# Kernel tuning notes

Hardware: AMD Instinct MI355X
Metric: run time of the kernel (lower is better)

Reference implementation:

```python
import jax, jax.numpy as jnp
import numpy as np

B, C, V, K, H, W = 1, 3, 9, 8, 512, 512


def setup_inputs() -> dict:
    key = jax.random.key(0)
    k0, k1 = jax.random.split(key, 2)
    x = jax.random.normal(k0, (B, C, K, H, W), jnp.float32)          # FDL layers (spatial)
    y_views = jax.random.normal(k1, (B, C, V, H, W), jnp.float32)    # observed views (spatial)
    g = jnp.arange(3, dtype=jnp.float32) - 1.0                       # 3x3 camera grid positions
    uu, vv = jnp.meshgrid(g, g, indexing='ij')
    u = uu.reshape(-1)
    v = vv.reshape(-1)
    d = jnp.linspace(-2.0, 2.0, K).astype(jnp.float32)               # d_fdl disparities
    rho = jnp.full((1,), 0.3, jnp.float32)
    return {"x": x, "y_views": y_views, "u": u, "v": v, "d": d, "rho": rho}


def _pack_half_spectrum(Xf, x_c, y_c, n_proc):
    # [..., H, W] -> transpose to [..., W, H], center-roll so zero freq is at (x_c-1, y_c-1),
    # flatten x-major, keep the non-redundant half spectrum (first n_proc entries).
    Xt = jnp.swapaxes(Xf, -1, -2)
    Xt = jnp.roll(Xt, shift=(x_c - 1, y_c - 1), axis=(-2, -1))
    sh = Xt.shape
    return Xt.reshape(sh[:-2] + (sh[-2] * sh[-1],))[..., :n_proc]


def reference(x, y_views, u, v, d, rho):
    Bn, Cn, Kn = x.shape[0], x.shape[1], x.shape[2]
    Hn, Wn = x.shape[-2], x.shape[-1]
    rho = rho.reshape(())
    x_c = (Wn + 2) // 2                      # ceil((W+1)/2)
    y_c = (Hn + 2) // 2
    n_proc = Hn * (x_c - 1) + y_c            # half-spectrum size
    e0 = 1 - Hn % 2
    e1 = 1 - Wn % 2

    X = jnp.fft.fft2(x)                      # [B,C,K,H,W] complex64
    Y = jnp.fft.fft2(y_views)                # [B,C,V,H,W] complex64
    Xp = jnp.moveaxis(_pack_half_spectrum(X, x_c, y_c, n_proc), 2, 3) * rho   # [B,C,F,K]
    Yp = jnp.moveaxis(_pack_half_spectrum(Y, x_c, y_c, n_proc), 2, 3)         # [B,C,F,V]

    # centered angular frequency grids, flattened x-major to match packing order
    wx = (jnp.arange(Wn, dtype=jnp.float32) - (x_c - 1)) * (2.0 * np.pi / Wn)
    wy = (jnp.arange(Hn, dtype=jnp.float32) - (y_c - 1)) * (2.0 * np.pi / Hn)
    wx_f = jnp.repeat(wx, Hn)[:n_proc]       # [F]
    wy_f = jnp.tile(wy, Wn)[:n_proc]         # [F]

    # FDL data matrix A[f,v,k] = exp(i * d_k * (u_v*wx_f + v_v*wy_f))
    shift = u[None, :] * wx_f[:, None] + v[None, :] * wy_f[:, None]   # [F,V]
    A = jnp.exp(1j * shift[:, :, None] * d[None, None, :])            # [F,V,K] complex64
    Ah = jnp.conj(A)
    ATA = jnp.einsum('fvk,fvl->fkl', Ah, A)                           # [F,K,K]
    ATb = jnp.einsum('fvk,bcfv->bcfk', Ah, Yp)                        # [B,C,F,K]
    M = ATA + rho * jnp.eye(Kn, dtype=ATA.dtype)
    fdl = jnp.linalg.solve(M, (ATb + Xp)[..., None])[..., 0]          # [B,C,F,K]

    # pad redundant half with zeros, restore [B,C,K,H,W] layout
    fdl = jnp.pad(fdl, ((0, 0), (0, 0), (0, Hn * Wn - n_proc), (0, 0)))
    fdl = fdl.reshape(Bn, Cn, Wn, Hn, Kn).transpose(0, 1, 4, 3, 2)    # [B,C,K,H,W]

    # Hermitian (conjugate) symmetry reconstruction
    fdl = fdl.at[..., y_c:, x_c - 1:].set(jnp.conj(fdl[..., e0:y_c - 1, e1:x_c][..., ::-1, ::-1]))
    fdl = fdl.at[..., e0:y_c, x_c:].set(jnp.conj(fdl[..., y_c - 1:, e1:x_c - 1][..., ::-1, ::-1]))
    fdl = jnp.roll(fdl, shift=(1 - y_c, 1 - x_c), axis=(-2, -1))
    return jnp.fft.ifft2(fdl).real
```

## Files before the change

kernel.cpp:

```cpp
#include <hip/hip_runtime.h>
#include <math.h>

constexpr int N    = 512;
constexpr int LOGN = 9;
constexpr int NN   = N * N;
constexpr int CCH  = 3;
constexpr int KK   = 8;
constexpr int VV   = 9;
constexpr int FHALF = N * (N / 2) + (N / 2 + 1);
constexpr float PI_F = 3.14159265358979323846f;

__device__ __forceinline__ float2 cmulf(float2 a, float2 b) {
    return make_float2(a.x * b.x - a.y * b.y, a.x * b.y + a.y * b.x);
}
__device__ __forceinline__ float2 cadd(float2 a, float2 b) { return make_float2(a.x + b.x, a.y + b.y); }
__device__ __forceinline__ float2 csub(float2 a, float2 b) { return make_float2(a.x - b.x, a.y - b.y); }

template<int SG>
__device__ __forceinline__ float2 cmuli(float2 z) {
    return (SG < 0) ? make_float2(z.y, -z.x) : make_float2(-z.y, z.x);
}

template<int SG>
__device__ __forceinline__ void dft8(float2 x[8]) {
    const float c = 0.70710678118654752440f;
    float2 a0 = cadd(x[0], x[4]), a1 = cadd(x[1], x[5]);
    float2 a2 = cadd(x[2], x[6]), a3 = cadd(x[3], x[7]);
    float2 d0 = csub(x[0], x[4]), d1 = csub(x[1], x[5]);
    float2 d2 = csub(x[2], x[6]), d3 = csub(x[3], x[7]);
    float2 b0 = d0;
    float2 b1 = cmulf(d1, make_float2(c, (float)SG * c));
    float2 b2 = cmuli<SG>(d2);
    float2 b3 = cmulf(d3, make_float2(-c, (float)SG * c));
    float2 aa0 = cadd(a0, a2), aa1 = cadd(a1, a3);
    float2 ab0 = csub(a0, a2), ab1 = cmuli<SG>(csub(a1, a3));
    float2 ba0 = cadd(b0, b2), ba1 = cadd(b1, b3);
    float2 bb0 = csub(b0, b2), bb1 = cmuli<SG>(csub(b1, b3));
    x[0] = cadd(aa0, aa1); x[4] = csub(aa0, aa1);
    x[2] = cadd(ab0, ab1); x[6] = csub(ab0, ab1);
    x[1] = cadd(ba0, ba1); x[5] = csub(ba0, ba1);
    x[3] = cadd(bb0, bb1); x[7] = csub(bb0, bb1);
}

__device__ __forceinline__ void twiddle8(float2 v[8], float base) {
    float sn, cs;
    __sincosf(base, &sn, &cs);
    float2 w1 = make_float2(cs, sn);
    float2 wk = w1;
    v[1] = cmulf(v[1], wk);
    #pragma unroll
    for (int k = 2; k < 8; ++k) { wk = cmulf(wk, w1); v[k] = cmulf(v[k], wk); }
}

template<int SG>
__device__ __forceinline__ void wave_fft512(float2 v[8], float* sre, float* sim,
                                            int t, int stride, int off) {
    int t1 = t >> 3, t0 = t & 7;
    dft8<SG>(v);
    twiddle8(v, (float)SG * (2.0f * PI_F / 512.0f) * (float)t);
    #pragma unroll
    for (int k = 0; k < 8; ++k) {
        int a = (68 * k + 8 * t1 + t0) * stride + off;
        sre[a] = v[k].x; sim[a] = v[k].y;
    }
    #pragma unroll
    for (int n = 0; n < 8; ++n) {
        int a = (68 * t1 + 8 * n + t0) * stride + off;
        v[n] = make_float2(sre[a], sim[a]);
    }
    dft8<SG>(v);
    twiddle8(v, (float)SG * (2.0f * PI_F / 64.0f) * (float)t0);
    #pragma unroll
    for (int k = 0; k < 8; ++k) {
        int a = (68 * t0 + 8 * k + t1) * stride + off;
        sre[a] = v[k].x; sim[a] = v[k].y;
    }
    #pragma unroll
    for (int n = 0; n < 8; ++n) {
        int a = (68 * n + 8 * t0 + t1) * stride + off;
        v[n] = make_float2(sre[a], sim[a]);
    }
    dft8<SG>(v);
}

__global__ __launch_bounds__(256) void k_fft_r2c_rows_pack(const float* __restrict__ inx,
                                                           const float* __restrict__ iny,
                                                           int nximg,
                                                           float2* __restrict__ out) {
    __shared__ float sre[4][544];
    __shared__ float sim[4][544];
    int w = threadIdx.x >> 6, t = threadIdx.x & 63;
    long long gp = (long long)blockIdx.x * 4 + w;
    long long row0 = gp * 2;
    long long xrows = (long long)nximg * N;
    const float* src0 = (row0 < xrows) ? (inx + row0 * N)
                                       : (iny + (row0 - xrows) * N);
    const float* src1 = src0 + N;
    float2 v[8];
    #pragma unroll
    for (int e = 0; e < 8; ++e) v[e] = make_float2(src0[t + 64 * e], src1[t + 64 * e]);
    wave_fft512<-1>(v, sre[w], sim[w], t, 1, 0);
    int kb = (t >> 3) + 8 * (t & 7);
    #pragma unroll
    for (int k0 = 0; k0 < 8; ++k0) {
        int p = kb + 64 * k0;
        sre[w][p] = v[k0].x; sim[w][p] = v[k0].y;
    }
    float2* dst0 = out + row0 * N;
    float2* dst1 = dst0 + N;
    #pragma unroll
    for (int k0 = 4; k0 < 8; ++k0) {
        int p  = kb + 64 * k0;
        int mp = 512 - p;
        float zmx = sre[w][mp], zmy = sim[w][mp];
        float2 Zp = v[k0];
        dst0[p] = make_float2(0.5f * (Zp.x + zmx), 0.5f * (Zp.y - zmy));
        dst1[p] = make_float2(0.5f * (Zp.y + zmy), 0.5f * (zmx - Zp.x));
    }
    if (t == 0) {
        dst0[0] = make_float2(v[0].x, 0.0f);
        dst1[0] = make_float2(v[0].y, 0.0f);
    }
}

__global__ __launch_bounds__(256) void k_fft_r2c_rows(const float* __restrict__ in,
                                                      float2* __restrict__ out) {
    __shared__ float sre[4][544];
    __shared__ float sim[4][544];
    int w = threadIdx.x >> 6, t = threadIdx.x & 63;
    long long grow = (long long)blockIdx.x * 4 + w;
    const float* src = in + grow * N;
    float2 v[8];
    #pragma unroll
    for (int e = 0; e < 8; ++e) v[e] = make_float2(src[t + 64 * e], 0.0f);
    wave_fft512<-1>(v, sre[w], sim[w], t, 1, 0);
    float2* dst = out + grow * N;
    int kb = (t >> 3) + 8 * (t & 7);
    #pragma unroll
    for (int k0 = 0; k0 < 8; ++k0) dst[kb + 64 * k0] = v[k0];
}

template<int SG>
__global__ __launch_bounds__(256) void k_fft_pairswap(float2* __restrict__ data,
                                                      float scale, int lex, int sex) {
    __shared__ float sre[4][544];
    __shared__ float sim[4][544];
    int w = threadIdx.x >> 6, t = threadIdx.x & 63;
    int b = blockIdx.x;
    long long imgBase = (long long)(b >> 7) * NN;
    int pa = (b & 127) << 1;
    int rowg = pa + (w & 1) + ((w >> 1) << 8);
    const float2* src = data + imgBase + (long long)rowg * N;
    float2 v[8];
    #pragma unroll
    for (int e = 0; e < 8; ++e) v[e] = src[t + 64 * (e ^ lex)];
    __syncthreads();
    wave_fft512<SG>(v, sre[w], sim[w], t, 1, 0);
    float2* dst = data + imgBase + (long long)(rowg ^ 256) * N;
    int kb = (t >> 3) + 8 * (t & 7);
    #pragma unroll
    for (int k0 = 0; k0 < 8; ++k0) {
        float2 z = v[k0];
        dst[kb + 64 * (k0 ^ sex)] = make_float2(z.x * scale, z.y * scale);
    }
}

__global__ __launch_bounds__(256) void k_fft_cols_fwd(const float2* __restrict__ in,
                                                      float2* __restrict__ out) {
    __shared__ float tre[4896];
    __shared__ float tim[4896];
    int t = threadIdx.x;
    long long imgOff = (long long)blockIdx.y * NN;
    int bx = blockIdx.x;
    int x0 = bx ? (248 + (bx << 3)) : 0;
    {
        int xi2 = (t & 3) << 1;
        int yb  = t >> 2;
        const float2* img = in + imgOff;
        #pragma unroll
        for (int it = 0; it < 8; ++it) {
            int y = it * 64 + yb;
            float4 q = *(const float4*)&img[(long long)y * N + x0 + xi2];
            int a = y * 9 + xi2;
            tre[a] = q.x; tim[a] = q.y; tre[a + 1] = q.z; tim[a + 1] = q.w;
        }
    }
    __syncthreads();
    int w = t >> 6, lane = t & 63;
    int kb = (lane >> 3) + 8 * (lane & 7);
    #pragma unroll
    for (int r = 0; r < 2; ++r) {
        int cc = (w << 1) | r;
        if (bx == 0 && cc != 0) continue;
        float2 v[8];
        #pragma unroll
        for (int e = 0; e < 8; ++e) {
            int a = (lane + 64 * e) * 9 + cc;
            v[e] = make_float2(tre[a], tim[a]);
        }
        wave_fft512<-1>(v, tre, tim, lane, 9, cc);
        #pragma unroll
        for (int k0 = 0; k0 < 8; ++k0) {
            int a = (kb + 64 * k0) * 9 + cc;
            tre[a] = v[k0].x; tim[a] = v[k0].y;
        }
    }
    __syncthreads();
    {
        int xi = t >> 5, co = t & 31;
        if (!(bx == 0 && xi != 0)) {
            float2* orow = out + imgOff + (long long)((x0 + xi) ^ 256) * N;
            #pragma unroll
            for (int it = 0; it < 8; ++it) {
                int b = it * 64 + co * 2;
                int y1 = b ^ 256;
                int a1 = y1 * 9 + xi, a2 = (y1 + 1) * 9 + xi;
                *(float4*)&orow[b] = make_float4(tre[a1], tim[a1], tre[a2], tim[a2]);
            }
        }
    }
}

__device__ __forceinline__ void accum_pair(float2 bacc[KK], float tr[KK], float s,
                                           float d0, float dlt, float2 Yp, float2 Yn) {
    float2 Sp = make_float2(Yp.x + Yn.x, Yp.y + Yn.y);
    float2 Dm = make_float2(Yp.x - Yn.x, Yp.y - Yn.y);
    float sn, cs;
    __sincosf(s * d0, &sn, &cs);  float2 p = make_float2(cs, sn);
    __sincosf(s * dlt, &sn, &cs); float2 q = make_float2(cs, sn);
    float2 w = q;
    #pragma unroll
    for (int k = 0; k < KK; ++k) {
        bacc[k].x += p.x * Sp.x + p.y * Dm.y;
        bacc[k].y += p.x * Sp.y - p.y * Dm.x;
        if (k < KK - 1) {
            p = cmulf(p, q);
            tr[k + 1] += 2.0f * w.x;
            w = cmulf(w, q);
        }
    }
}

__device__ __forceinline__ void solve_point(float2 bacc[KK], float tr[KK], float rho) {
    float diag = tr[0] + rho;
    float L[36], Li[KK];
    #pragma unroll
    for (int j = 0; j < KK; ++j) {
        float acc = diag;
        #pragma unroll
        for (int t = 0; t < j; ++t) { float l = L[(j * (j - 1)) / 2 + t]; acc -= l * l; }
        float dj = sqrtf(acc);
        float inv = 1.0f / dj;
        Li[j] = inv;
        #pragma unroll
        for (int i = j + 1; i < KK; ++i) {
            float a = tr[i - j];
            #pragma unroll
            for (int t = 0; t < j; ++t)
                a -= L[(i * (i - 1)) / 2 + t] * L[(j * (j - 1)) / 2 + t];
            L[(i * (i - 1)) / 2 + j] = a * inv;
        }
    }
    #pragma unroll
    for (int i = 0; i < KK; ++i) {
        float2 a = bacc[i];
        #pragma unroll
        for (int t = 0; t < i; ++t) {
            float l = L[(i * (i - 1)) / 2 + t];
            a.x -= l * bacc[t].x;
            a.y -= l * bacc[t].y;
        }
        bacc[i] = make_float2(a.x * Li[i], a.y * Li[i]);
    }
    #pragma unroll
    for (int i = KK - 1; i >= 0; --i) {
        float2 a = bacc[i];
        #pragma unroll
        for (int t = i + 1; t < KK; ++t) {
            float l = L[(t * (t - 1)) / 2 + i];
            a.x -= l * bacc[t].x;
            a.y -= l * bacc[t].y;
        }
        bacc[i] = make_float2(a.x * Li[i], a.y * Li[i]);
    }
}

__global__ __launch_bounds__(256) void k_solve_ifft(const float2* __restrict__ Xs,
                                                    const float2* __restrict__ Ys,
                                                    float2* __restrict__ P,
                                                    float2* __restrict__ S0,
                                                    const float* __restrict__ uu,
                                                    const float* __restrict__ vv,
                                                    const float* __restrict__ dd,
                                                    const float* __restrict__ rhop) {
    __shared__ float gre[KK][N];
    __shared__ float gim[KK][N];
    __shared__ float fsre[4][544];
    __shared__ float fsim[4][544];
    int a  = blockIdx.x;
    int ch = blockIdx.y;
    int t  = threadIdx.x;
    float rho = rhop[0];
    float d0 = dd[0], dlt = dd[1] - dd[0];
    const float C = 2.0f * PI_F / (float)N;
    float wxv = (float)(a - 256) * C;
    const float2* Xrow = Xs + (long long)ch * KK * NN + (long long)a * N;
    const float2* Yrow = Ys + (long long)ch * VV * NN + (long long)a * N;
    float wy0 = (float)(t - 256) * C;
    float wy1 = (float)(t)       * C;

    float2 bacc0[KK], bacc1[KK];
    float tr0[KK], tr1[KK];
    {
        const float2* Yc = Yrow + (long long)4 * NN;
        float2 yc0 = Yc[t], yc1 = Yc[t + 256];
        #pragma unroll
        for (int k = 0; k < KK; ++k) { bacc0[k] = yc0; bacc1[k] = yc1; }
        tr0[0] = tr1[0] = (float)VV;
        #pragma unroll
        for (int l = 1; l < KK; ++l) { tr0[l] = 1.0f; tr1[l] = 1.0f; }
    }
    #pragma unroll
    for (int j = 0; j < 4; ++j) {
        int vp = 5 + j, vn = 3 - j;
        float su = uu[vp], sv = vv[vp];
        const float2* Ypr = Yrow + (long long)vp * NN;
        const float2* Ynr = Yrow + (long long)vn * NN;
        float2 Yp0 = Ypr[t], Yn0 = Ynr[t];
        float2 Yp1 = Ypr[t + 256], Yn1 = Ynr[t + 256];
        accum_pair(bacc0, tr0, su * wxv + sv * wy0, d0, dlt, Yp0, Yn0);
        accum_pair(bacc1, tr1, su * wxv + sv * wy1, d0, dlt, Yp1, Yn1);
    }
    #pragma unroll
    for (int k = 0; k < KK; ++k) {
        const float2* Xr = Xrow + (long long)k * NN;
        float2 x0v = Xr[t], x1v = Xr[t + 256];
        bacc0[k].x += rho * x0v.x; bacc0[k].y += rho * x0v.y;
        bacc1[k].x += rho * x1v.x; bacc1[k].y += rho * x1v.y;
    }
    solve_point(bacc0, tr0, rho);
    solve_point(bacc1, tr1, rho);
    #pragma unroll
    for (int k = 0; k < KK; ++k) {
        gre[k][t] = bacc0[k].x;       gim[k][t] = bacc0[k].y;
        gre[k][t + 256] = bacc1[k].x; gim[k][t + 256] = bacc1[k].y;
    }
    __syncthreads();
    if (a == 256 && t >= 1) {
        int b = t + 256, bs = 256 - t;
        #pragma unroll
        for (int k = 0; k < KK; ++k) {
            gre[k][b] = gre[k][bs];
            gim[k][b] = -gim[k][bs];
        }
    }
    __syncthreads();

    int w = t >> 6, lane = t & 63;
    int kb = (lane >> 3) + 8 * (lane & 7);
    const float inv512 = 1.0f / 512.0f;
    #pragma unroll
    for (int r = 0; r < 2; ++r) {
        int k = (w << 1) | r;
        float2 v[8];
        #pragma unroll
        for (int e = 0; e < 8; ++e) {
            int idx = (lane + 64 * e) ^ 256;
            v[e] = make_float2(gre[k][idx], gim[k][idx]);
        }
        wave_fft512<1>(v, fsre[w], fsim[w], lane, 1, 0);
        float s0x = gre[k][0], s0y = gim[k][0];
        if (lane == 0)
            S0[(long long)(ch * KK + k) * 257 + a] =
                make_float2(s0x * inv512, s0y * inv512);
        float2* Pimg = P + (long long)(ch * KK + k) * NN;
        int prow = (a >= 1 && a <= 255) ? (a + 256) : (a == 0 ? 256 : 0);
        float2* pmain = Pimg + (long long)prow * N;
        #pragma unroll
        for (int k0 = 0; k0 < 8; ++k0) {
            int pos = kb + 64 * k0;
            float2 W = v[k0];
            pmain[pos] = make_float2(W.x * inv512, W.y * inv512);
        }
    }
}

__global__ __launch_bounds__(256) void k_fft_cols_inv_real(const float2* __restrict__ in,
                                                           const float2* __restrict__ T0,
                                                           float* __restrict__ out,
                                                           float scale) {
    __shared__ float tre[4896];
    __shared__ float tim[4896];
    int t = threadIdx.x;
    long long imgOff = (long long)blockIdx.y * NN;
    int b0 = blockIdx.x << 3;
    {
        int xi2 = (t & 3) << 1;
        int yb  = t >> 2;
        const float2* img = in + imgOff;
        const float2* T0i = T0 + (long long)blockIdx.y * 257;
        #pragma unroll
        for (int it = 0; it < 4; ++it) {
            int p = 256 + it * 64 + yb;
            float4 q = *(const float4*)&img[(long long)p * N + b0 + xi2];
            int c = p * 9 + xi2;
            tre[c] = q.x; tim[c] = q.y; tre[c + 1] = q.z; tim[c + 1] = q.w;
            if (p > 256) {
                float2 t0 = T0i[p - 256];
                int m0 = b0 + xi2;
                float sg0 = (m0 & 1) ? -1.0f : 1.0f;
                float sg1 = -sg0;
                int cm = (512 - p) * 9 + xi2;
                tre[cm]     = q.x - t0.x * sg0;
                tim[cm]     = -q.y + t0.y * sg0;
                tre[cm + 1] = q.z - t0.x * sg1;
                tim[cm + 1] = -q.w + t0.y * sg1;
            }
        }
        if (t < 4) {
            int xi2b = t << 1;
            float4 q = *(const float4*)&img[(long long)(b0 + xi2b)];
            tre[xi2b] = q.x; tim[xi2b] = q.y; tre[xi2b + 1] = q.z; tim[xi2b + 1] = q.w;
        }
    }
    __syncthreads();
    int w = t >> 6, lane = t & 63;
    int kb = (lane >> 3) + 8 * (lane & 7);
    #pragma unroll
    for (int r = 0; r < 2; ++r) {
        int cc = (w << 1) | r;
        float2 v[8];
        #pragma unroll
        for (int e = 0; e < 8; ++e) {
            int a = (lane + 64 * e) * 9 + cc;
            v[e] = make_float2(tre[a], tim[a]);
        }
        wave_fft512<1>(v, tre, tim, lane, 9, cc);
        #pragma unroll
        for (int k0 = 0; k0 < 8; ++k0)
            tre[(kb + 64 * k0) * 9 + cc] = v[k0].x;
    }
    __syncthreads();
    {
        int xi = t >> 5, co = t & 31;
        float* orow = out + (long long)blockIdx.y * NN + (long long)(b0 + xi) * N;
        #pragma unroll
        for (int it = 0; it < 4; ++it) {
            int ww = it * 128 + co * 4;
            *(float4*)&orow[ww] = make_float4(tre[ww * 9 + xi] * scale,
                                              tre[(ww + 1) * 9 + xi] * scale,
                                              tre[(ww + 2) * 9 + xi] * scale,
                                              tre[(ww + 3) * 9 + xi] * scale);
        }
    }
}

__global__ __launch_bounds__(256) void k_transpose_inplace(float2* __restrict__ data) {
    int ti = blockIdx.x, tj = blockIdx.y;
    if (ti > tj) return;
    float2* img = data + (long long)blockIdx.z * NN;
    __shared__ float2 ta[32][33];
    __shared__ float2 tb[32][33];
    int tx = threadIdx.x, ty = threadIdx.y;
    int r0 = ti << 5, c0 = tj << 5;
    bool diag = (ti == tj);
    #pragma unroll
    for (int kk = 0; kk < 4; ++kk) {
        int r = ty + (kk << 3);
        ta[r][tx] = img[(long long)(r0 + r) * N + (c0 + tx)];
        if (!diag) tb[r][tx] = img[(long long)(c0 + r) * N + (r0 + tx)];
    }
    __syncthreads();
    #pragma unroll
    for (int kk = 0; kk < 4; ++kk) {
        int r = ty + (kk << 3);
        img[(long long)(c0 + r) * N + (r0 + tx)] = ta[tx][r];
        if (!diag) img[(long long)(r0 + r) * N + (c0 + tx)] = tb[tx][r];
    }
}

__global__ __launch_bounds__(256) void k_fft_c2r_rows(const float2* __restrict__ in,
                                                      float* __restrict__ out, float scale) {
    __shared__ float sre[4][544];
    __shared__ float sim[4][544];
    int w = threadIdx.x >> 6, t = threadIdx.x & 63;
    long long grow = (long long)blockIdx.x * 4 + w;
    const float2* src = in + grow * N;
    float2 v[8];
    #pragma unroll
    for (int e = 0; e < 8; ++e) v[e] = src[t + 64 * e];
    wave_fft512<1>(v, sre[w], sim[w], t, 1, 0);
    float* dst = out + grow * N;
    int kb = (t >> 3) + 8 * (t & 7);
    #pragma unroll
    for (int k0 = 0; k0 < 8; ++k0) dst[kb + 64 * k0] = v[k0].x * scale;
}

__global__ __launch_bounds__(256) void k_solve(float2* __restrict__ Xs,
                                               const float2* __restrict__ Ys,
                                               const float* __restrict__ uu,
                                               const float* __restrict__ vv,
                                               const float* __restrict__ dd,
                                               const float* __restrict__ rhop) {
    int f = blockIdx.x * 256 + threadIdx.x;
    if (f >= FHALF) return;
    long long coffX = (long long)blockIdx.y * KK * NN;
    long long coffY = (long long)blockIdx.y * VV * NN;
    float rho = rhop[0];
    int x = f >> LOGN;
    int y = f & (N - 1);
    float wxv = (float)(x - N / 2) * (2.0f * PI_F / (float)N);
    float wyv = (float)(y - N / 2) * (2.0f * PI_F / (float)N);
    float d0 = dd[0], dlt = dd[1] - dd[0];
    float2 bacc[KK];
    float tr[KK];
    {
        float2 Yc = Ys[coffY + (long long)4 * NN + f];
        #pragma unroll
        for (int k = 0; k < KK; ++k) bacc[k] = Yc;
        tr[0] = (float)VV;
        #pragma unroll
        for (int l = 1; l < KK; ++l) tr[l] = 1.0f;
    }
    #pragma unroll
    for (int j = 0; j < 4; ++j) {
        int vp = 5 + j, vn = 3 - j;
        float s = uu[vp] * wxv + vv[vp] * wyv;
        accum_pair(bacc, tr, s, d0, dlt,
                   Ys[coffY + (long long)vp * NN + f],
                   Ys[coffY + (long long)vn * NN + f]);
    }
    #pragma unroll
    for (int k = 0; k < KK; ++k) {
        float2 Xk = Xs[coffX + (long long)k * NN + f];
        bacc[k].x += rho * Xk.x;
        bacc[k].y += rho * Xk.y;
    }
    solve_point(bacc, tr, rho);
    int xm = (N - x) & (N - 1);
    int ym = (N - y) & (N - 1);
    long long fm = (long long)xm * N + ym;
    bool conjMirror = false, zeroMirror = false;
    if (x >= 1 && x <= N / 2 - 1) {
        if (y == 0) zeroMirror = true; else conjMirror = true;
    } else if (x == N / 2 && y >= 1 && y <= N / 2 - 1) {
        conjMirror = true;
    }
    #pragma unroll
    for (int k = 0; k < KK; ++k) {
        float2* base = Xs + coffX + (long long)k * NN;
        float2 z = bacc[k];
        base[f] = z;
        if (conjMirror)      base[fm] = make_float2(z.x, -z.y);
        else if (zeroMirror) base[fm] = make_float2(0.f, 0.f);
    }
}

extern "C" void kernel_launch(void* const* d_in, const int* in_sizes, int n_in,
                              void* d_out, int out_size, void* d_ws, size_t ws_size,
                              hipStream_t stream) {
    (void)in_sizes; (void)n_in; (void)out_size;
    const float* x   = (const float*)d_in[0];
    const float* yv  = (const float*)d_in[1];
    const float* uu  = (const float*)d_in[2];
    const float* vvp = (const float*)d_in[3];
    const float* dd  = (const float*)d_in[4];
    const float* rho = (const float*)d_in[5];
    float* out = (float*)d_out;
    float2* ws = (float2*)d_ws;

    const size_t s0Elems = (size_t)CCH * KK * 257;
    const size_t needBatchedPack =
        (size_t)2 * CCH * (KK + VV) * NN * sizeof(float2) + s0Elems * sizeof(float2);
    const size_t needChanPack =
        (size_t)2 * (KK + VV) * NN * sizeof(float2) + (size_t)KK * 257 * sizeof(float2);
    const float invN = 1.0f / (float)N;

    if (ws_size >= needChanPack) {
        bool batched = ws_size >= needBatchedPack;
        int iters = batched ? 1 : CCH;
        int ncs   = batched ? CCH : 1;
        int nx = ncs * KK, ny = ncs * VV;
        for (int it = 0; it < iters; ++it) {
            float2* Xt = ws;
            float2* Yt = ws + (size_t)nx * NN;
            float2* Rt = ws + (size_t)(nx + ny) * NN;
            float2* S0 = ws + (size_t)2 * (nx + ny) * NN;
            const float* xin = x  + (size_t)it * KK * NN;
            const float* yin = yv + (size_t)it * VV * NN;
            float* oout = out + (size_t)it * KK * NN;
            k_fft_r2c_rows_pack<<<(nx + ny) * (N / 8), 256, 0, stream>>>(xin, yin, nx, Rt);
            k_fft_cols_fwd<<<dim3(33, nx + ny), 256, 0, stream>>>(Rt, Xt);
            k_solve_ifft<<<dim3(257, ncs), 256, 0, stream>>>(Xt, Yt, Rt, S0, uu, vvp, dd, rho);
            k_fft_cols_inv_real<<<dim3(N / 8, nx), 256, 0, stream>>>(Rt, S0, oout, invN);
        }
    } else {
        for (int it = 0; it < CCH; ++it) {
            float2* Xb = ws;
            float2* Yb = ws + (size_t)KK * NN;
            const float* xin = x  + (size_t)it * KK * NN;
            const float* yin = yv + (size_t)it * VV * NN;
            float* oout = out + (size_t)it * KK * NN;
            k_fft_r2c_rows<<<KK * (N / 4), 256, 0, stream>>>(xin, Xb);
            k_fft_r2c_rows<<<VV * (N / 4), 256, 0, stream>>>(yin, Yb);
            k_transpose_inplace<<<dim3(16, 16, KK), dim3(32, 8), 0, stream>>>(Xb);
            k_transpose_inplace<<<dim3(16, 16, VV), dim3(32, 8), 0, stream>>>(Yb);
            k_fft_pairswap<-1><<<KK * (N / 4), 256, 0, stream>>>(Xb, 1.0f, 0, 4);
            k_fft_pairswap<-1><<<VV * (N / 4), 256, 0, stream>>>(Yb, 1.0f, 0, 4);
            k_solve<<<dim3((FHALF + 255) / 256, 1), 256, 0, stream>>>(Xb, Yb, uu, vvp, dd, rho);
            k_fft_pairswap<1><<<KK * (N / 4), 256, 0, stream>>>(Xb, invN, 4, 0);
            k_transpose_inplace<<<dim3(16, 16, KK), dim3(32, 8), 0, stream>>>(Xb);
            k_fft_c2r_rows<<<KK * (N / 4), 256, 0, stream>>>(Xb, oout, invN);
        }
    }
}
```

Before: 172.9 us.

## Transpose half-spectrum in row FFT so column FFTs read contiguous lines

The row r2c FFT kernel now stages each block's 8 rows of half-spectrum output in shared memory and writes them transposed into a compact [257 x 512] per-image layout. The column FFT becomes a simple per-wave line FFT over contiguous memory instead of a tiled kernel with a strided shared-memory gather. This is meant to cut the strided column gather and the shared-memory transposition cost in the forward column pass. In exchange, the row kernel does a scattered transposed store of 8 consecutive float2 per row segment and needs an extra block barrier.

```diff
diff --git a/kernel.cpp b/kernel.cpp
--- a/kernel.cpp
+++ b/kernel.cpp
@@ -8,6 +8,7 @@
 constexpr int KK   = 8;
 constexpr int VV   = 9;
 constexpr int FHALF = N * (N / 2) + (N / 2 + 1);
+constexpr int NS   = 257;
 constexpr float PI_F = 3.14159265358979323846f;
 
 __device__ __forceinline__ float2 cmulf(float2 a, float2 b) {
@@ -83,44 +84,88 @@
     dft8<SG>(v);
 }
 
-__global__ __launch_bounds__(256) void k_fft_r2c_rows_pack(const float* __restrict__ inx,
-                                                           const float* __restrict__ iny,
-                                                           int nximg,
-                                                           float2* __restrict__ out) {
-    __shared__ float sre[4][544];
-    __shared__ float sim[4][544];
+__global__ __launch_bounds__(256) void k_fft_r2c_rows_pack_T(const float* __restrict__ inx,
+                                                             const float* __restrict__ iny,
+                                                             int nximg,
+                                                             float2* __restrict__ outT) {
+    __shared__ float ure[2313];
+    __shared__ float uim[2313];
     int w = threadIdx.x >> 6, t = threadIdx.x & 63;
-    long long gp = (long long)blockIdx.x * 4 + w;
-    long long row0 = gp * 2;
+    int blk = blockIdx.x;
+    int img = blk >> 6;
+    int rowbase = (blk & 63) << 3;
+    long long row0 = (long long)blk * 8 + 2 * w;
     long long xrows = (long long)nximg * N;
     const float* src0 = (row0 < xrows) ? (inx + row0 * N)
                                        : (iny + (row0 - xrows) * N);
     const float* src1 = src0 + N;
+    float* sre = ure + w * 544;
+    float* sim = uim + w * 544;
     float2 v[8];
     #pragma unroll
     for (int e = 0; e < 8; ++e) v[e] = make_float2(src0[t + 64 * e], src1[t + 64 * e]);
-    wave_fft512<-1>(v, sre[w], sim[w], t, 1, 0);
+    wave_fft512<-1>(v, sre, sim, t, 1, 0);
     int kb = (t >> 3) + 8 * (t & 7);
     #pragma unroll
     for (int k0 = 0; k0 < 8; ++k0) {
         int p = kb + 64 * k0;
-        sre[w][p] = v[k0].x; sim[w][p] = v[k0].y;
-    }
-    float2* dst0 = out + row0 * N;
-    float2* dst1 = dst0 + N;
+        sre[p] = v[k0].x; sim[p] = v[k0].y;
+    }
+    float2 r0v[4], r1v[4];
     #pragma unroll
     for (int k0 = 4; k0 < 8; ++k0) {
         int p  = kb + 64 * k0;
         int mp = 512 - p;
-        float zmx = sre[w][mp], zmy = sim[w][mp];
+        float zmx = sre[mp], zmy = sim[mp];
         float2 Zp = v[k0];
-        dst0[p] = make_float2(0.5f * (Zp.x + zmx), 0.5f * (Zp.y - zmy));
-        dst1[p] = make_float2(0.5f * (Zp.y + zmy), 0.5f * (zmx - Zp.x));
+        r0v[k0 - 4] = make_float2(0.5f * (Zp.x + zmx), 0.5f * (Zp.y - zmy));
+        r1v[k0 - 4] = make_float2(0.5f * (Zp.y + zmy), 0.5f * (zmx - Zp.x));
+    }
+    float2 z0 = v[0];
+    __syncthreads();
+    #pragma unroll
+    for (int k0 = 0; k0 < 4; ++k0) {
+        int s = kb + 64 * k0;
+        ure[s * 9 + 2 * w]     = r0v[k0].x; uim[s * 9 + 2 * w]     = r0v[k0].y;
+        ure[s * 9 + 2 * w + 1] = r1v[k0].x; uim[s * 9 + 2 * w + 1] = r1v[k0].y;
     }
     if (t == 0) {
-        dst0[0] = make_float2(v[0].x, 0.0f);
-        dst1[0] = make_float2(v[0].y, 0.0f);
-    }
+        ure[256 * 9 + 2 * w]     = z0.x; uim[256 * 9 + 2 * w]     = 0.0f;
+        ure[256 * 9 + 2 * w + 1] = z0.y; uim[256 * 9 + 2 * w + 1] = 0.0f;
+    }
+    __syncthreads();
+    float2* dst = outT + (long long)img * (NS * N);
+    int tt = threadIdx.x;
+    int r = tt & 7;
+    #pragma unroll
+    for (int j = 0; j < 8; ++j) {
+        int s = j * 32 + (tt >> 3);
+        dst[s * N + rowbase + r] = make_float2(ure[s * 9 + r], uim[s * 9 + r]);
+    }
+    if (tt < 8)
+        dst[256 * N + rowbase + tt] = make_float2(ure[256 * 9 + tt], uim[256 * 9 + tt]);
+}
+
+__global__ __launch_bounds__(256) void k_fft_cols_lin(const float2* __restrict__ inT,
+                                                      float2* __restrict__ out,
+                                                      int nlines) {
+    __shared__ float sre[4][544];
+    __shared__ float sim[4][544];
+    int w = threadIdx.x >> 6, t = threadIdx.x & 63;
+    int l = blockIdx.x * 4 + w;
+    if (l >= nlines) return;
+    int img = l / NS;
+    int s   = l - img * NS;
+    const float2* src = inT + (long long)img * (NS * N) + (long long)s * N;
+    float2 v[8];
+    #pragma unroll
+    for (int e = 0; e < 8; ++e) v[e] = src[t + 64 * e];
+    wave_fft512<-1>(v, sre[w], sim[w], t, 1, 0);
+    int outrow = (s == 256) ? 256 : s;
+    float2* dst = out + (long long)img * NN + (long long)outrow * N;
+    int kb = (t >> 3) + 8 * (t & 7);
+    #pragma unroll
+    for (int k0 = 0; k0 < 8; ++k0) dst[kb + 64 * (k0 ^ 4)] = v[k0];
 }
 
 __global__ __launch_bounds__(256) void k_fft_r2c_rows(const float* __restrict__ in,
@@ -162,62 +207,6 @@
     for (int k0 = 0; k0 < 8; ++k0) {
         float2 z = v[k0];
         dst[kb + 64 * (k0 ^ sex)] = make_float2(z.x * scale, z.y * scale);
-    }
-}
-
-__global__ __launch_bounds__(256) void k_fft_cols_fwd(const float2* __restrict__ in,
-                                                      float2* __restrict__ out) {
-    __shared__ float tre[4896];
-    __shared__ float tim[4896];
-    int t = threadIdx.x;
-    long long imgOff = (long long)blockIdx.y * NN;
-    int bx = blockIdx.x;
-    int x0 = bx ? (248 + (bx << 3)) : 0;
-    {
-        int xi2 = (t & 3) << 1;
-        int yb  = t >> 2;
-        const float2* img = in + imgOff;
-        #pragma unroll
-        for (int it = 0; it < 8; ++it) {
-            int y = it * 64 + yb;
-            float4 q = *(const float4*)&img[(long long)y * N + x0 + xi2];
-            int a = y * 9 + xi2;
-            tre[a] = q.x; tim[a] = q.y; tre[a + 1] = q.z; tim[a + 1] = q.w;
-        }
-    }
-    __syncthreads();
-    int w = t >> 6, lane = t & 63;
-    int kb = (lane >> 3) + 8 * (lane & 7);
-    #pragma unroll
-    for (int r = 0; r < 2; ++r) {
-        int cc = (w << 1) | r;
-        if (bx == 0 && cc != 0) continue;
-        float2 v[8];
-        #pragma unroll
-        for (int e = 0; e < 8; ++e) {
-            int a = (lane + 64 * e) * 9 + cc;
-            v[e] = make_float2(tre[a], tim[a]);
-        }
-        wave_fft512<-1>(v, tre, tim, lane, 9, cc);
-        #pragma unroll
-        for (int k0 = 0; k0 < 8; ++k0) {
-            int a = (kb + 64 * k0) * 9 + cc;
-            tre[a] = v[k0].x; tim[a] = v[k0].y;
-        }
-    }
-    __syncthreads();
-    {
-        int xi = t >> 5, co = t & 31;
-        if (!(bx == 0 && xi != 0)) {
-            float2* orow = out + imgOff + (long long)((x0 + xi) ^ 256) * N;
-            #pragma unroll
-            for (int it = 0; it < 8; ++it) {
-                int b = it * 64 + co * 2;
-                int y1 = b ^ 256;
-                int a1 = y1 * 9 + xi, a2 = (y1 + 1) * 9 + xi;
-                *(float4*)&orow[b] = make_float4(tre[a1], tim[a1], tre[a2], tim[a2]);
-            }
-        }
     }
 }
 
@@ -589,8 +578,9 @@
             const float* xin = x  + (size_t)it * KK * NN;
             const float* yin = yv + (size_t)it * VV * NN;
             float* oout = out + (size_t)it * KK * NN;
-            k_fft_r2c_rows_pack<<<(nx + ny) * (N / 8), 256, 0, stream>>>(xin, yin, nx, Rt);
-            k_fft_cols_fwd<<<dim3(33, nx + ny), 256, 0, stream>>>(Rt, Xt);
+            int nlines = (nx + ny) * NS;
+            k_fft_r2c_rows_pack_T<<<(nx + ny) * 64, 256, 0, stream>>>(xin, yin, nx, Rt);
+            k_fft_cols_lin<<<(nlines + 3) / 4, 256, 0, stream>>>(Rt, Xt, nlines);
             k_solve_ifft<<<dim3(257, ncs), 256, 0, stream>>>(Xt, Yt, Rt, S0, uu, vvp, dd, rho);
             k_fft_cols_inv_real<<<dim3(N / 8, nx), 256, 0, stream>>>(Rt, S0, oout, invN);
         }
```

After: 168.4 us. 2.6% less time.
